# Optimization experiments

Hardware: AMD Instinct MI355X
Metric: run time of the kernel (lower is better)

## Reference

```python
import jax, jax.numpy as jnp
import numpy as np

# config matching init_kwargs
B = 16
NEI = 30
S1 = 2 * NEI + 1          # 61: image side, also local attn window size
KS = 3
SZ = 2 * KS + 1           # 7: conv kernel size
PCH = SZ * SZ             # 49 conv out channels
D = 128                   # d_model
H = 8                     # heads (all local, since n_local_attn_heads == heads)
DH = D // H               # 16
L = 4                     # depth
S = S1 * S1               # 3721 sequence length
NW = S // S1              # 61 windows of size 61
WIN = S1
POS = 4096
FF = 4 * D
EPS = 1e-5


def _sincos(n, d):
    pos = np.arange(n)[:, None].astype(np.float64)
    i = np.arange(d)[None, :]
    ang = pos / np.power(10000.0, 2 * (i // 2) / d)
    tab = np.zeros((n, d))
    tab[:, 0::2] = np.sin(ang[:, 0::2])
    tab[:, 1::2] = np.cos(ang[:, 1::2])
    return jnp.asarray(tab, jnp.float32)


def _ln(x, s, b):
    m = x.mean(-1, keepdims=True)
    v = ((x - m) ** 2).mean(-1, keepdims=True)
    return (x - m) / jnp.sqrt(v + EPS) * s + b


def _local_mask():
    # valid-key mask per window over [prev | self | next] blocks; edges padded
    ones = jnp.ones((NW, WIN), jnp.float32)
    p = jnp.pad(ones, ((1, 1), (0, 0)))
    return jnp.concatenate([p[:-2], p[1:-1], p[2:]], axis=1) > 0.5


def _local_attn(x, wq, wk, wv, wo, wob):
    # non-causal windowed attention, look_backward=1, look_forward=1 (lucidrains LocalAttention)
    bq = x.shape[0]

    def to_windows(w):
        y = (x @ w).reshape(bq, S, H, DH).transpose(0, 2, 1, 3)
        return y.reshape(bq * H, NW, WIN, DH)

    q = to_windows(wq) * (DH ** -0.5)
    k = to_windows(wk)
    v = to_windows(wv)

    def gather(t):
        p = jnp.pad(t, ((0, 0), (1, 1), (0, 0), (0, 0)))
        return jnp.concatenate([p[:, :-2], p[:, 1:-1], p[:, 2:]], axis=2)

    bk, bv = gather(k), gather(v)
    scores = jnp.einsum('bnqd,bnkd->bnqk', q, bk)
    scores = jnp.where(_local_mask()[None, :, None, :], scores, -1e9)
    attn = jax.nn.softmax(scores, axis=-1)
    o = jnp.einsum('bnqk,bnkd->bnqd', attn, bv)
    o = o.reshape(bq, H, S, DH).transpose(0, 2, 1, 3).reshape(bq, S, D)
    return o @ wo + wob


def _forward(x, conv_w, conv_b, lt_w, lt_b, pos_table, ln1_s, ln1_b, wq, wk, wv, wo, wo_b,
             ln2_s, ln2_b, ff_w1, ff_b1, ff_w2, ff_b2, pre_w1, pre_b1, pre_w2, pre_b2):
    # conv patch extraction, 'same' padding, ReLU
    p = jax.lax.conv_general_dilated(x[:, None], conv_w, (1, 1), [(KS, KS), (KS, KS)],
                                     dimension_numbers=('NCHW', 'OIHW', 'NCHW'))
    p = jax.nn.relu(p + conv_b[None, :, None, None])
    p = p.reshape(B, PCH, S).transpose(0, 2, 1)       # [B, S, 49]
    h = p @ lt_w + lt_b + pos_table[:S][None]         # [B, S, D]
    for i in range(L):
        h = h + _local_attn(_ln(h, ln1_s[i], ln1_b[i]), wq[i], wk[i], wv[i], wo[i], wo_b[i])
        hn = _ln(h, ln2_s[i], ln2_b[i])
        h = h + (jax.nn.gelu(hn @ ff_w1[i] + ff_b1[i], approximate=False) @ ff_w2[i] + ff_b2[i])
    out = jax.nn.relu(h @ pre_w1 + pre_b1) @ pre_w2 + pre_b2  # [B, S, 1]
    return out.reshape(B, S1, S1)


def setup_inputs() -> dict:
    key = jax.random.key(0)
    ks = jax.random.split(key, 12)
    g = lambda k, sh, sc=0.02: jax.random.normal(k, sh, jnp.float32) * sc
    return {
        'x': jax.random.normal(ks[0], (B, S1, S1), jnp.float32),
        'conv_w': g(ks[1], (PCH, 1, SZ, SZ), 0.1),
        'conv_b': jnp.zeros((PCH,), jnp.float32),
        'lt_w': g(ks[2], (PCH, D)),
        'lt_b': jnp.zeros((D,), jnp.float32),
        'pos_table': _sincos(POS, D),
        'ln1_s': jnp.ones((L, D), jnp.float32), 'ln1_b': jnp.zeros((L, D), jnp.float32),
        'wq': g(ks[3], (L, D, D)), 'wk': g(ks[4], (L, D, D)), 'wv': g(ks[5], (L, D, D)),
        'wo': g(ks[6], (L, D, D)), 'wo_b': jnp.zeros((L, D), jnp.float32),
        'ln2_s': jnp.ones((L, D), jnp.float32), 'ln2_b': jnp.zeros((L, D), jnp.float32),
        'ff_w1': g(ks[7], (L, D, FF)), 'ff_b1': jnp.zeros((L, FF), jnp.float32),
        'ff_w2': g(ks[8], (L, FF, D)), 'ff_b2': jnp.zeros((L, D), jnp.float32),
        'pre_w1': g(ks[9], (D, D)), 'pre_b1': jnp.zeros((D,), jnp.float32),
        'pre_w2': g(ks[10], (D, 1)), 'pre_b2': jnp.zeros((1,), jnp.float32),
    }


def reference(x, conv_w, conv_b, lt_w, lt_b, pos_table, ln1_s, ln1_b, wq, wk, wv, wo, wo_b,
              ln2_s, ln2_b, ff_w1, ff_b1, ff_w2, ff_b2, pre_w1, pre_b1, pre_w2, pre_b2):
    return _forward(x, conv_w, conv_b, lt_w, lt_b, pos_table, ln1_s, ln1_b, wq, wk, wv, wo, wo_b,
                    ln2_s, ln2_b, ff_w1, ff_b1, ff_w2, ff_b2, pre_w1, pre_b1, pre_w2, pre_b2)
```

## Files before the change

kernel.cpp:

```cpp
#include <hip/hip_runtime.h>
#include <hip/hip_bf16.h>
#include <math.h>
#include <string.h>

#define B_   16
#define S1_  61
#define S_   3721
#define D_   128
#define H_   8
#define NW_  61
#define FF_  512
#define BS_  (B_*S_)

#define SC_LOG2E 0.36067376022224085f

typedef unsigned int   uint32;
typedef unsigned short ushort16;
typedef __attribute__((ext_vector_type(8))) short  short8;
typedef __attribute__((ext_vector_type(4))) float  floatx4;
typedef __attribute__((ext_vector_type(4))) uint32 uint32x4;

__device__ __forceinline__ ushort16 f2bf(float f) {
  uint32 u = __float_as_uint(f);
  uint32 r = u + 0x7fffu + ((u >> 16) & 1u);
  return (ushort16)(r >> 16);
}
__device__ __forceinline__ uint32 pkbf(float a, float b) {
  __hip_bfloat162 t = __float22bfloat162_rn(float2{a, b});
  uint32 r;
  memcpy(&r, &t, 4);
  return r;
}
__device__ __forceinline__ short8 mk8(uint32 a, uint32 b) {
  uint32x4 v = {a, b, 0u, 0u};
  return __builtin_bit_cast(short8, v);
}
__device__ __forceinline__ void gl2lds16(const void* g, void* l) {
  __builtin_amdgcn_global_load_lds(
      (const __attribute__((address_space(1))) unsigned int*)g,
      (__attribute__((address_space(3))) unsigned int*)l, 16, 0, 0);
}

__global__ __launch_bounds__(256) void prep_w(
    const float* __restrict__ wq, const float* __restrict__ wk, const float* __restrict__ wv,
    const float* __restrict__ wo, const float* __restrict__ w1, const float* __restrict__ w2,
    const float* __restrict__ lt, const float* __restrict__ pw1,
    const float* __restrict__ cw, const float* __restrict__ cb,
    ushort16* __restrict__ qkv_t, ushort16* __restrict__ wo_t, ushort16* __restrict__ w1_t,
    ushort16* __restrict__ w2_t, ushort16* __restrict__ lt_t, ushort16* __restrict__ pw1_t,
    ushort16* __restrict__ wc_t, float* __restrict__ cb_pad) {
  int i = blockIdx.x * 256 + threadIdx.x;
  if (i < 196608) {
    int l = i / 49152, r = i % 49152;
    int n = r / 128, k = r % 128;
    const float* src = (n < 128) ? wq : (n < 256) ? wk : wv;
    qkv_t[i] = f2bf(src[(l * 128 + k) * 128 + (n & 127)]);
  } else if (i < 262144) {
    int j = i - 196608;
    int l = j / 16384, r = j % 16384;
    int n = r / 128, k = r % 128;
    wo_t[j] = f2bf(wo[(l * 128 + k) * 128 + n]);
  } else if (i < 524288) {
    int j = i - 262144;
    int l = j / 65536, r = j % 65536;
    int n = r / 128, k = r % 128;
    w1_t[j] = f2bf(w1[(size_t)l * 65536 + k * 512 + n]);
  } else if (i < 786432) {
    int j = i - 524288;
    int l = j / 65536, r = j % 65536;
    int n = r / 512, k = r % 512;
    w2_t[j] = f2bf(w2[(size_t)l * 65536 + k * 128 + n]);
  } else if (i < 794624) {
    int j = i - 786432;
    int n = j / 64, k = j % 64;
    lt_t[j] = f2bf(k < 49 ? lt[k * 128 + n] : 0.f);
  } else if (i < 811008) {
    int j = i - 794624;
    int n = j / 128, k = j % 128;
    pw1_t[j] = f2bf(pw1[k * 128 + n]);
  } else if (i < 815104) {
    int j = i - 811008;
    int n = j >> 6, k = j & 63;
    wc_t[j] = f2bf((n < 49 && k < 49) ? cw[n * 49 + k] : 0.f);
  } else if (i < 815168) {
    int j = i - 815104;
    cb_pad[j] = (j < 49) ? cb[j] : 0.f;
  }
}

__global__ __launch_bounds__(256) void im2col_k(const float* __restrict__ x,
                                                ushort16* __restrict__ X) {
  int t = blockIdx.x * 256 + threadIdx.x;
  if (t >= BS_ * 64) return;
  int tap = t & 63;
  int row = t >> 6;
  if (tap >= 49) { X[t] = 0; return; }
  int b = row / S_, s = row % S_;
  int i = s / S1_, j = s % S1_;
  int di = tap / 7, dj = tap % 7;
  int ii = i + di - 3, jj = j + dj - 3;
  float v = 0.f;
  if ((unsigned)ii < (unsigned)S1_ && (unsigned)jj < (unsigned)S1_)
    v = x[(b * S1_ + ii) * S1_ + jj];
  X[t] = f2bf(v);
}

enum { E_BF16 = 0, E_H0 = 1, E_RES = 2, E_GELU = 3, E_RELU = 4, E_RESBF = 5, E_QKV = 6 };

template <int EPI, int K>
__global__ __launch_bounds__(512) void gemm_bf16(
    const ushort16* __restrict__ A, int lda,
    const ushort16* __restrict__ Bt, int ldbt,
    float* __restrict__ H,
    ushort16* __restrict__ Cb, int ldc,
    const float* __restrict__ bias,
    const float* __restrict__ pos,
    int M, int N) {
  __shared__ ushort16 As[8192];
  __shared__ ushort16 Bs[8192];
  int bm = blockIdx.y * 128, bn = blockIdx.x * 128;
  int tid = threadIdx.x;
  int lane = tid & 63, wave = tid >> 6;
  int wm = (wave >> 1) * 32, wn = (wave & 1) * 64;
  int ln = lane & 15, qd = lane >> 4;
  int lr = lane >> 3;
  int cg = (lane & 7) ^ lr;

  const ushort16* aP[2];
  const ushort16* bP[2];
  #pragma unroll
  for (int u = 0; u < 2; u++) {
    int s = wave * 2 + u;
    int ar = bm + s * 8 + lr; if (ar > M - 1) ar = M - 1;
    int br = bn + s * 8 + lr; if (br > N - 1) br = N - 1;
    aP[u] = A  + (size_t)ar * lda  + cg * 8;
    bP[u] = Bt + (size_t)br * ldbt + cg * 8;
  }

  floatx4 acc[2][4] = {};
  #pragma unroll
  for (int kc = 0; kc < K; kc += 64) {
    #pragma unroll
    for (int u = 0; u < 2; u++) {
      int s = wave * 2 + u;
      gl2lds16(aP[u] + kc, &As[s * 512]);
      gl2lds16(bP[u] + kc, &Bs[s * 512]);
    }
    __syncthreads();
    #pragma unroll
    for (int ks = 0; ks < 64; ks += 32) {
      int cb0 = ks >> 3;
      short8 af[2], bf[4];
      #pragma unroll
      for (int i = 0; i < 2; i++) {
        int row = wm + i * 16 + ln;
        af[i] = *(const short8*)&As[row * 64 + (((cb0 + qd) ^ (ln & 7)) * 8)];
      }
      #pragma unroll
      for (int j = 0; j < 4; j++) {
        int row = wn + j * 16 + ln;
        bf[j] = *(const short8*)&Bs[row * 64 + (((cb0 + qd) ^ (ln & 7)) * 8)];
      }
      #pragma unroll
      for (int i = 0; i < 2; i++)
        #pragma unroll
        for (int j = 0; j < 4; j++)
          acc[i][j] = __builtin_amdgcn_mfma_f32_16x16x32_bf16(af[i], bf[j], acc[i][j], 0, 0, 0);
    }
    if (kc + 64 < K) __syncthreads();
  }

  float qsc = (EPI == E_QKV && bn == 0) ? SC_LOG2E : 1.0f;
  #pragma unroll
  for (int i = 0; i < 2; i++) {
    #pragma unroll
    for (int r = 0; r < 4; r++) {
      int gm = bm + wm + i * 16 + qd * 4 + r;
      if (gm >= M) continue;
      #pragma unroll
      for (int j = 0; j < 4; j++) {
        int gn = bn + wn + j * 16 + ln;
        if (gn >= N) continue;
        float v = acc[i][j][r];
        if (EPI == E_BF16) {
          Cb[(size_t)gm * ldc + gn] = f2bf(v);
        } else if (EPI == E_QKV) {
          Cb[(size_t)gm * ldc + gn] = f2bf(v * qsc);
        } else if (EPI == E_H0) {
          H[(size_t)gm * 128 + gn] = v + bias[gn] + pos[(size_t)(gm % S_) * 128 + gn];
        } else if (EPI == E_RES) {
          size_t o = (size_t)gm * 128 + gn;
          H[o] += v + bias[gn];
        } else if (EPI == E_GELU) {
          float g = v + bias[gn];
          g = 0.5f * g * (1.f + erff(g * 0.70710678118654752f));
          Cb[(size_t)gm * ldc + gn] = f2bf(g);
        } else if (EPI == E_RELU) {
          float g = fmaxf(v + bias[gn], 0.f);
          Cb[(size_t)gm * ldc + gn] = f2bf(g);
        } else if (EPI == E_RESBF) {
          size_t o = (size_t)gm * 128 + gn;
          float g = H[o] + v + bias[gn];
          H[o] = g;
          Cb[(size_t)gm * ldc + gn] = f2bf(g);
        }
      }
    }
  }
}

__global__ __launch_bounds__(256) void ln_bf16(const float* __restrict__ x,
                                               ushort16* __restrict__ y,
                                               const float* __restrict__ g,
                                               const float* __restrict__ bta,
                                               int rows) {
  int wv = (blockIdx.x * 256 + threadIdx.x) >> 6;
  int lane = threadIdx.x & 63;
  if (wv >= rows) return;
  const float* xr = x + (size_t)wv * D_;
  float x0 = xr[lane], x1 = xr[lane + 64];
  float sum = x0 + x1;
  #pragma unroll
  for (int off = 32; off; off >>= 1) sum += __shfl_xor(sum, off);
  float mean = sum * (1.f / 128.f);
  float d0 = x0 - mean, d1 = x1 - mean;
  float vs = d0 * d0 + d1 * d1;
  #pragma unroll
  for (int off = 32; off; off >>= 1) vs += __shfl_xor(vs, off);
  float inv = rsqrtf(vs * (1.f / 128.f) + 1e-5f);
  ushort16* yr = y + (size_t)wv * D_;
  yr[lane]      = f2bf(d0 * inv * g[lane]      + bta[lane]);
  yr[lane + 64] = f2bf(d1 * inv * g[lane + 64] + bta[lane + 64]);
}

__global__ __launch_bounds__(64) void attn3(const ushort16* __restrict__ qkv,
                                            ushort16* __restrict__ o) {
  int bid = blockIdx.x;
  int xcd = bid & 7, idx = bid >> 3;
  int w  = idx % NW_;
  int bh = xcd * 16 + idx / NW_;
  int hh = bh & 7, b = bh >> 3;
  __shared__ ushort16 Kl[192][16];
  __shared__ ushort16 Vl[192][16];
  int lane = threadIdx.x;
  int qcol = lane & 15, quad = lane >> 4;

  #pragma unroll
  for (int c = 0; c < 6; c++) {
    int e = c * 64 + lane;
    int j = e >> 1, half = (e & 1) * 8;
    int krow = (w - 1) * 61 + j;
    if (krow < 0) krow = 0;
    if (krow > S_ - 1) krow = S_ - 1;
    const ushort16* gk = qkv + ((size_t)(b * S_ + krow) * 384 + 128 + hh * 16 + half);
    gl2lds16(gk,       &Kl[0][0] + c * 512);
    gl2lds16(gk + 128, &Vl[0][0] + c * 512);
  }

  short8 qf[4];
  #pragma unroll
  for (int qt = 0; qt < 4; qt++) {
    int qloc = qt * 16 + qcol;
    if (qloc > 60) qloc = 60;
    const uint32* qp = (const uint32*)(qkv + ((size_t)(b * S_ + w * 61 + qloc) * 384 + hh * 16 + quad * 4));
    qf[qt] = mk8(qp[0], qp[1]);
  }
  __syncthreads();

  int j0 = (w == 0) ? 61 : 0;
  int j1 = (w == NW_ - 1) ? 122 : 183;
  int kt0 = (w == 0) ? 3 : 0;
  int kt1 = (w == NW_ - 1) ? 8 : 12;

  floatx4 oacc[4];
  #pragma unroll
  for (int qt = 0; qt < 4; qt++) { oacc[qt][0]=0.f; oacc[qt][1]=0.f; oacc[qt][2]=0.f; oacc[qt][3]=0.f; }
  float lsum[4] = {0.f, 0.f, 0.f, 0.f};
  const floatx4 zero4 = {0.f, 0.f, 0.f, 0.f};

  for (int kt = kt0; kt < kt1; kt++) {
    const uint32* kp = (const uint32*)&Kl[kt * 16 + qcol][quad * 4];
    short8 kf = mk8(kp[0], kp[1]);

    int kb = kt * 16 + quad * 4;
    uint32 va = (uint32)Vl[kb + 0][qcol] | ((uint32)Vl[kb + 1][qcol] << 16);
    uint32 vb = (uint32)Vl[kb + 2][qcol] | ((uint32)Vl[kb + 3][qcol] << 16);
    short8 vf = mk8(va, vb);

    floatx4 sacc[4];
    #pragma unroll
    for (int qt = 0; qt < 4; qt++)
      sacc[qt] = __builtin_amdgcn_mfma_f32_16x16x32_bf16(kf, qf[qt], zero4, 0, 0, 0);

    uint32 m01 = (((unsigned)(kb + 0 - j0) < (unsigned)(j1 - j0)) ? 0x0000ffffu : 0u)
               | (((unsigned)(kb + 1 - j0) < (unsigned)(j1 - j0)) ? 0xffff0000u : 0u);
    uint32 m23 = (((unsigned)(kb + 2 - j0) < (unsigned)(j1 - j0)) ? 0x0000ffffu : 0u)
               | (((unsigned)(kb + 3 - j0) < (unsigned)(j1 - j0)) ? 0xffff0000u : 0u);
    #pragma unroll
    for (int qt = 0; qt < 4; qt++) {
      float e0 = __builtin_amdgcn_exp2f(sacc[qt][0]);
      float e1 = __builtin_amdgcn_exp2f(sacc[qt][1]);
      float e2 = __builtin_amdgcn_exp2f(sacc[qt][2]);
      float e3 = __builtin_amdgcn_exp2f(sacc[qt][3]);
      uint32 p01 = pkbf(e0, e1) & m01;
      uint32 p23 = pkbf(e2, e3) & m23;
      lsum[qt] += (__uint_as_float(p01 << 16) + __uint_as_float(p01 & 0xffff0000u))
                + (__uint_as_float(p23 << 16) + __uint_as_float(p23 & 0xffff0000u));
      oacc[qt] = __builtin_amdgcn_mfma_f32_16x16x32_bf16(mk8(p01, p23), vf, oacc[qt], 0, 0, 0);
    }
  }

  #pragma unroll
  for (int qt = 0; qt < 4; qt++) {
    float l = lsum[qt];
    l += __shfl_xor(l, 16);
    l += __shfl_xor(l, 32);
    lsum[qt] = 1.0f / fmaxf(l, 1e-30f);
  }
  #pragma unroll
  for (int qt = 0; qt < 4; qt++) {
    #pragma unroll
    for (int r = 0; r < 4; r++) {
      int qloc = qt * 16 + quad * 4 + r;
      float invl = __shfl(lsum[qt], quad * 4 + r);
      if (qloc < 61) {
        size_t row = (size_t)b * S_ + w * 61 + qloc;
        o[row * 128 + hh * 16 + qcol] = f2bf(oacc[qt][r] * invl);
      }
    }
  }
}

__global__ __launch_bounds__(256) void head2(const ushort16* __restrict__ t2,
                                             const float* __restrict__ w2,
                                             const float* __restrict__ b2,
                                             float* __restrict__ out, int rows) {
  int wv = (blockIdx.x * 256 + threadIdx.x) >> 6;
  int lane = threadIdx.x & 63;
  if (wv >= rows) return;
  uint32 u = *(const uint32*)(t2 + (size_t)wv * 128 + lane * 2);
  float a = __uint_as_float(u << 16) * w2[lane * 2]
          + __uint_as_float(u & 0xffff0000u) * w2[lane * 2 + 1];
  #pragma unroll
  for (int off = 32; off; off >>= 1) a += __shfl_xor(a, off);
  if (lane == 0) out[wv] = a + b2[0];
}

extern "C" void kernel_launch(void* const* d_in, const int* in_sizes, int n_in,
                              void* d_out, int out_size, void* d_ws, size_t ws_size,
                              hipStream_t stream) {
  const float* x      = (const float*)d_in[0];
  const float* conv_w = (const float*)d_in[1];
  const float* conv_b = (const float*)d_in[2];
  const float* lt_w   = (const float*)d_in[3];
  const float* lt_b   = (const float*)d_in[4];
  const float* pos    = (const float*)d_in[5];
  const float* ln1_s  = (const float*)d_in[6];
  const float* ln1_b  = (const float*)d_in[7];
  const float* wq     = (const float*)d_in[8];
  const float* wk     = (const float*)d_in[9];
  const float* wv     = (const float*)d_in[10];
  const float* wo     = (const float*)d_in[11];
  const float* wo_b   = (const float*)d_in[12];
  const float* ln2_s  = (const float*)d_in[13];
  const float* ln2_b  = (const float*)d_in[14];
  const float* ff_w1  = (const float*)d_in[15];
  const float* ff_b1  = (const float*)d_in[16];
  const float* ff_w2  = (const float*)d_in[17];
  const float* ff_b2  = (const float*)d_in[18];
  const float* pre_w1 = (const float*)d_in[19];
  const float* pre_b1 = (const float*)d_in[20];
  const float* pre_w2 = (const float*)d_in[21];
  const float* pre_b2 = (const float*)d_in[22];

  char* ws = (char*)d_ws;
  const size_t SZ_H   = (size_t)BS_ * 128 * 4;
  const size_t SZ_HN  = (size_t)BS_ * 128 * 2;
  const size_t SZ_QKV = (size_t)BS_ * 384 * 2;
  const size_t SZ_O   = (size_t)BS_ * 128 * 2;
  float*    h    = (float*)ws;
  ushort16* hn   = (ushort16*)(ws + SZ_H);
  ushort16* qkvb = (ushort16*)(ws + SZ_H + SZ_HN);
  ushort16* ob   = (ushort16*)(ws + SZ_H + SZ_HN + SZ_QKV);
  char*     wsw  = ws + SZ_H + SZ_HN + SZ_QKV + SZ_O;
  ushort16* qkv_t = (ushort16*)(wsw);
  ushort16* wo_t  = qkv_t + 196608;
  ushort16* w1_t  = wo_t  + 65536;
  ushort16* w2_t  = w1_t  + 262144;
  ushort16* lt_t  = w2_t  + 262144;
  ushort16* pw1_t = lt_t  + 8192;
  ushort16* wc_t  = pw1_t + 16384;
  float*    cb_pad = (float*)(wc_t + 4096);
  ushort16* X  = ob;
  ushort16* p  = qkvb;
  ushort16* t  = qkvb;
  ushort16* hb = hn;
  ushort16* t2 = ob;

  prep_w<<<dim3(3185), 256, 0, stream>>>(wq, wk, wv, wo, ff_w1, ff_w2, lt_w, pre_w1,
                                         conv_w, conv_b,
                                         qkv_t, wo_t, w1_t, w2_t, lt_t, pw1_t, wc_t, cb_pad);
  im2col_k<<<dim3((BS_ * 64 + 255) / 256), 256, 0, stream>>>(x, X);

  const int MB = (BS_ + 127) / 128;
  int lnBlocks = (BS_ + 3) / 4;
  gemm_bf16<E_RELU, 64><<<dim3(1, MB), 512, 0, stream>>>(X, 64, wc_t, 64, nullptr, p, 64,
                                                         cb_pad, nullptr, BS_, 64);
  gemm_bf16<E_H0, 64><<<dim3(1, MB), 512, 0, stream>>>(p, 64, lt_t, 64, h, nullptr, 128,
                                                       lt_b, pos, BS_, 128);

  for (int l = 0; l < 4; l++) {
    ln_bf16<<<dim3(lnBlocks), 256, 0, stream>>>(h, hn, ln1_s + l * 128, ln1_b + l * 128, BS_);
    gemm_bf16<E_QKV, 128><<<dim3(3, MB), 512, 0, stream>>>(hn, 128, qkv_t + (size_t)l * 49152, 128,
                                                           nullptr, qkvb, 384, nullptr, nullptr,
                                                           BS_, 384);
    attn3<<<dim3(B_ * H_ * NW_), 64, 0, stream>>>(qkvb, ob);
    gemm_bf16<E_RES, 128><<<dim3(1, MB), 512, 0, stream>>>(ob, 128, wo_t + (size_t)l * 16384, 128,
                                                           h, nullptr, 128, wo_b + l * 128, nullptr,
                                                           BS_, 128);
    ln_bf16<<<dim3(lnBlocks), 256, 0, stream>>>(h, hn, ln2_s + l * 128, ln2_b + l * 128, BS_);
    gemm_bf16<E_GELU, 128><<<dim3(4, MB), 512, 0, stream>>>(hn, 128, w1_t + (size_t)l * 65536, 128,
                                                            nullptr, t, 512, ff_b1 + l * 512, nullptr,
                                                            BS_, 512);
    if (l < 3) {
      gemm_bf16<E_RES, 512><<<dim3(1, MB), 512, 0, stream>>>(t, 512, w2_t + (size_t)l * 65536, 512,
                                                             h, nullptr, 128, ff_b2 + l * 128, nullptr,
                                                             BS_, 128);
    } else {
      gemm_bf16<E_RESBF, 512><<<dim3(1, MB), 512, 0, stream>>>(t, 512, w2_t + (size_t)l * 65536, 512,
                                                               h, hb, 128, ff_b2 + l * 128, nullptr,
                                                               BS_, 128);
    }
  }
  gemm_bf16<E_RELU, 128><<<dim3(1, MB), 512, 0, stream>>>(hb, 128, pw1_t, 128,
                                                          nullptr, t2, 128, pre_b1, nullptr,
                                                          BS_, 128);
  head2<<<dim3(lnBlocks), 256, 0, stream>>>(t2, pre_w2, pre_b2, (float*)d_out, BS_);
}
```

Baseline: 811.6 us.

## Fuse LayerNorm into residual GEMM epilogues via cross-wave row statistics

Removes the standalone LayerNorm kernels by computing per-row sum and sum-of-squares in the epilogue of the GEMMs that write the residual stream (N=128), reducing across lanes with shuffles and across the two column waves through shared memory. The normalized bf16 activations are written directly, which saves eight launches and a full fp32 re-read of h per LN. In exchange it adds a block-wide sync in the epilogue, and the single-pass variance formula (E[x^2]-mean^2) is less numerically robust than the two-pass form it replaces.

```diff
diff --git a/kernel.cpp b/kernel.cpp
--- a/kernel.cpp
+++ b/kernel.cpp
@@ -105,7 +105,7 @@
   X[t] = f2bf(v);
 }
 
-enum { E_BF16 = 0, E_H0 = 1, E_RES = 2, E_GELU = 3, E_RELU = 4, E_RESBF = 5, E_QKV = 6 };
+enum { E_BF16 = 0, E_H0LN = 1, E_RESLN = 2, E_GELU = 3, E_RELU = 4, E_RESBF = 5, E_QKV = 6 };
 
 template <int EPI, int K>
 __global__ __launch_bounds__(512) void gemm_bf16(
@@ -115,9 +115,12 @@
     ushort16* __restrict__ Cb, int ldc,
     const float* __restrict__ bias,
     const float* __restrict__ pos,
+    const float* __restrict__ ls,
+    const float* __restrict__ lb,
     int M, int N) {
   __shared__ ushort16 As[8192];
   __shared__ ushort16 Bs[8192];
+  __shared__ float stats[128][2][2];
   int bm = blockIdx.y * 128, bn = blockIdx.x * 128;
   int tid = threadIdx.x;
   int lane = tid & 63, wave = tid >> 6;
@@ -170,67 +173,95 @@
     if (kc + 64 < K) __syncthreads();
   }
 
-  float qsc = (EPI == E_QKV && bn == 0) ? SC_LOG2E : 1.0f;
-  #pragma unroll
-  for (int i = 0; i < 2; i++) {
-    #pragma unroll
-    for (int r = 0; r < 4; r++) {
-      int gm = bm + wm + i * 16 + qd * 4 + r;
-      if (gm >= M) continue;
-      #pragma unroll
-      for (int j = 0; j < 4; j++) {
-        int gn = bn + wn + j * 16 + ln;
-        if (gn >= N) continue;
-        float v = acc[i][j][r];
-        if (EPI == E_BF16) {
-          Cb[(size_t)gm * ldc + gn] = f2bf(v);
-        } else if (EPI == E_QKV) {
-          Cb[(size_t)gm * ldc + gn] = f2bf(v * qsc);
-        } else if (EPI == E_H0) {
-          H[(size_t)gm * 128 + gn] = v + bias[gn] + pos[(size_t)(gm % S_) * 128 + gn];
-        } else if (EPI == E_RES) {
-          size_t o = (size_t)gm * 128 + gn;
-          H[o] += v + bias[gn];
-        } else if (EPI == E_GELU) {
-          float g = v + bias[gn];
-          g = 0.5f * g * (1.f + erff(g * 0.70710678118654752f));
-          Cb[(size_t)gm * ldc + gn] = f2bf(g);
-        } else if (EPI == E_RELU) {
-          float g = fmaxf(v + bias[gn], 0.f);
-          Cb[(size_t)gm * ldc + gn] = f2bf(g);
-        } else if (EPI == E_RESBF) {
-          size_t o = (size_t)gm * 128 + gn;
-          float g = H[o] + v + bias[gn];
-          H[o] = g;
-          Cb[(size_t)gm * ldc + gn] = f2bf(g);
+  if (EPI == E_H0LN || EPI == E_RESLN) {
+    float lsv[4], lbv[4];
+    #pragma unroll
+    for (int j = 0; j < 4; j++) {
+      int gn = wn + j * 16 + ln;
+      lsv[j] = ls[gn]; lbv[j] = lb[gn];
+    }
+    int wI = wn >> 6;
+    #pragma unroll
+    for (int i = 0; i < 2; i++) {
+      #pragma unroll
+      for (int r = 0; r < 4; r++) {
+        int lrow = wm + i * 16 + qd * 4 + r;
+        int gm = bm + lrow;
+        int gmc = (gm < M) ? gm : (M - 1);
+        float s1 = 0.f, s2 = 0.f;
+        #pragma unroll
+        for (int j = 0; j < 4; j++) {
+          int gn = wn + j * 16 + ln;
+          float v = acc[i][j][r];
+          float g;
+          if (EPI == E_H0LN) g = v + bias[gn] + pos[(size_t)(gmc % S_) * 128 + gn];
+          else               g = H[(size_t)gmc * 128 + gn] + v + bias[gn];
+          acc[i][j][r] = g;
+          if (gm < M) H[(size_t)gm * 128 + gn] = g;
+          s1 += g; s2 = fmaf(g, g, s2);
         }
-      }
-    }
-  }
-}
-
-__global__ __launch_bounds__(256) void ln_bf16(const float* __restrict__ x,
-                                               ushort16* __restrict__ y,
-                                               const float* __restrict__ g,
-                                               const float* __restrict__ bta,
-                                               int rows) {
-  int wv = (blockIdx.x * 256 + threadIdx.x) >> 6;
-  int lane = threadIdx.x & 63;
-  if (wv >= rows) return;
-  const float* xr = x + (size_t)wv * D_;
-  float x0 = xr[lane], x1 = xr[lane + 64];
-  float sum = x0 + x1;
-  #pragma unroll
-  for (int off = 32; off; off >>= 1) sum += __shfl_xor(sum, off);
-  float mean = sum * (1.f / 128.f);
-  float d0 = x0 - mean, d1 = x1 - mean;
-  float vs = d0 * d0 + d1 * d1;
-  #pragma unroll
-  for (int off = 32; off; off >>= 1) vs += __shfl_xor(vs, off);
-  float inv = rsqrtf(vs * (1.f / 128.f) + 1e-5f);
-  ushort16* yr = y + (size_t)wv * D_;
-  yr[lane]      = f2bf(d0 * inv * g[lane]      + bta[lane]);
-  yr[lane + 64] = f2bf(d1 * inv * g[lane + 64] + bta[lane + 64]);
+        #pragma unroll
+        for (int off = 1; off <= 8; off <<= 1) {
+          s1 += __shfl_xor(s1, off);
+          s2 += __shfl_xor(s2, off);
+        }
+        if (ln == 0) { stats[lrow][wI][0] = s1; stats[lrow][wI][1] = s2; }
+      }
+    }
+    __syncthreads();
+    #pragma unroll
+    for (int i = 0; i < 2; i++) {
+      #pragma unroll
+      for (int r = 0; r < 4; r++) {
+        int lrow = wm + i * 16 + qd * 4 + r;
+        int gm = bm + lrow;
+        if (gm >= M) continue;
+        float s1 = stats[lrow][0][0] + stats[lrow][1][0];
+        float s2 = stats[lrow][0][1] + stats[lrow][1][1];
+        float mean = s1 * (1.f / 128.f);
+        float var  = s2 * (1.f / 128.f) - mean * mean;
+        float inv  = rsqrtf(fmaxf(var, 0.f) + 1e-5f);
+        #pragma unroll
+        for (int j = 0; j < 4; j++) {
+          int gn = wn + j * 16 + ln;
+          Cb[(size_t)gm * 128 + gn] = f2bf((acc[i][j][r] - mean) * inv * lsv[j] + lbv[j]);
+        }
+      }
+    }
+  } else {
+    float qsc = (EPI == E_QKV && bn == 0) ? SC_LOG2E : 1.0f;
+    #pragma unroll
+    for (int i = 0; i < 2; i++) {
+      #pragma unroll
+      for (int r = 0; r < 4; r++) {
+        int gm = bm + wm + i * 16 + qd * 4 + r;
+        if (gm >= M) continue;
+        #pragma unroll
+        for (int j = 0; j < 4; j++) {
+          int gn = bn + wn + j * 16 + ln;
+          if (gn >= N) continue;
+          float v = acc[i][j][r];
+          if (EPI == E_BF16) {
+            Cb[(size_t)gm * ldc + gn] = f2bf(v);
+          } else if (EPI == E_QKV) {
+            Cb[(size_t)gm * ldc + gn] = f2bf(v * qsc);
+          } else if (EPI == E_GELU) {
+            float g = v + bias[gn];
+            g = 0.5f * g * (1.f + erff(g * 0.70710678118654752f));
+            Cb[(size_t)gm * ldc + gn] = f2bf(g);
+          } else if (EPI == E_RELU) {
+            float g = fmaxf(v + bias[gn], 0.f);
+            Cb[(size_t)gm * ldc + gn] = f2bf(g);
+          } else if (EPI == E_RESBF) {
+            size_t o = (size_t)gm * 128 + gn;
+            float g = H[o] + v + bias[gn];
+            H[o] = g;
+            Cb[(size_t)gm * ldc + gn] = f2bf(g);
+          }
+        }
+      }
+    }
+  }
 }
 
 __global__ __launch_bounds__(64) void attn3(const ushort16* __restrict__ qkv,
@@ -405,35 +436,34 @@
   const int MB = (BS_ + 127) / 128;
   int lnBlocks = (BS_ + 3) / 4;
   gemm_bf16<E_RELU, 64><<<dim3(1, MB), 512, 0, stream>>>(X, 64, wc_t, 64, nullptr, p, 64,
-                                                         cb_pad, nullptr, BS_, 64);
-  gemm_bf16<E_H0, 64><<<dim3(1, MB), 512, 0, stream>>>(p, 64, lt_t, 64, h, nullptr, 128,
-                                                       lt_b, pos, BS_, 128);
+                                                         cb_pad, nullptr, nullptr, nullptr, BS_, 64);
+  gemm_bf16<E_H0LN, 64><<<dim3(1, MB), 512, 0, stream>>>(p, 64, lt_t, 64, h, hn, 128,
+                                                         lt_b, pos, ln1_s, ln1_b, BS_, 128);
 
   for (int l = 0; l < 4; l++) {
-    ln_bf16<<<dim3(lnBlocks), 256, 0, stream>>>(h, hn, ln1_s + l * 128, ln1_b + l * 128, BS_);
     gemm_bf16<E_QKV, 128><<<dim3(3, MB), 512, 0, stream>>>(hn, 128, qkv_t + (size_t)l * 49152, 128,
                                                            nullptr, qkvb, 384, nullptr, nullptr,
-                                                           BS_, 384);
+                                                           nullptr, nullptr, BS_, 384);
     attn3<<<dim3(B_ * H_ * NW_), 64, 0, stream>>>(qkvb, ob);
-    gemm_bf16<E_RES, 128><<<dim3(1, MB), 512, 0, stream>>>(ob, 128, wo_t + (size_t)l * 16384, 128,
-                                                           h, nullptr, 128, wo_b + l * 128, nullptr,
-                                                           BS_, 128);
-    ln_bf16<<<dim3(lnBlocks), 256, 0, stream>>>(h, hn, ln2_s + l * 128, ln2_b + l * 128, BS_);
+    gemm_bf16<E_RESLN, 128><<<dim3(1, MB), 512, 0, stream>>>(ob, 128, wo_t + (size_t)l * 16384, 128,
+                                                             h, hn, 128, wo_b + l * 128, nullptr,
+                                                             ln2_s + l * 128, ln2_b + l * 128, BS_, 128);
     gemm_bf16<E_GELU, 128><<<dim3(4, MB), 512, 0, stream>>>(hn, 128, w1_t + (size_t)l * 65536, 128,
                                                             nullptr, t, 512, ff_b1 + l * 512, nullptr,
-                                                            BS_, 512);
+                                                            nullptr, nullptr, BS_, 512);
     if (l < 3) {
-      gemm_bf16<E_RES, 512><<<dim3(1, MB), 512, 0, stream>>>(t, 512, w2_t + (size_t)l * 65536, 512,
-                                                             h, nullptr, 128, ff_b2 + l * 128, nullptr,
-                                                             BS_, 128);
+      gemm_bf16<E_RESLN, 512><<<dim3(1, MB), 512, 0, stream>>>(t, 512, w2_t + (size_t)l * 65536, 512,
+                                                               h, hn, 128, ff_b2 + l * 128, nullptr,
+                                                               ln1_s + (l + 1) * 128, ln1_b + (l + 1) * 128,
+                                                               BS_, 128);
     } else {
       gemm_bf16<E_RESBF, 512><<<dim3(1, MB), 512, 0, stream>>>(t, 512, w2_t + (size_t)l * 65536, 512,
                                                                h, hb, 128, ff_b2 + l * 128, nullptr,
-                                                               BS_, 128);
+                                                               nullptr, nullptr, BS_, 128);
     }
   }
   gemm_bf16<E_RELU, 128><<<dim3(1, MB), 512, 0, stream>>>(hb, 128, pw1_t, 128,
                                                           nullptr, t2, 128, pre_b1, nullptr,
-                                                          BS_, 128);
+                                                          nullptr, nullptr, BS_, 128);
   head2<<<dim3(lnBlocks), 256, 0, stream>>>(t2, pre_w2, pre_b2, (float*)d_out, BS_);
 }
```

After: 732.1 us. 1.11x faster.
